# Kernel tuning notes

Hardware: AMD Instinct MI355X
Metric: run time of the kernel (lower is better)

Reference implementation:

```python
import jax, jax.numpy as jnp
import numpy as np

EPS = 1e-5

def conv1x1(x, w, b):
    # x: [B,C,H,W], w: [O,C], b: [O]
    return jnp.einsum('bchw,oc->bohw', x, w) + b[None, :, None, None]

def bn_eval(x, w, b, m, v):
    inv = w / jnp.sqrt(v + EPS)
    return (x - m[None, :, None, None]) * inv[None, :, None, None] + b[None, :, None, None]

def setup_inputs() -> dict:
    key = jax.random.key(0)
    ks = jax.random.split(key, 32)
    B, Fg, Fl, Fi, H, W = 4, 128, 128, 64, 64, 64
    d = {}
    d['g'] = jax.random.normal(ks[0], (B, Fg, H, W), jnp.float32)
    d['x'] = jax.random.normal(ks[1], (B, Fl, H, W), jnp.float32)
    d['wg_w'] = jax.random.normal(ks[2], (Fi, Fg), jnp.float32) * 0.1
    d['wg_b'] = jax.random.normal(ks[3], (Fi,), jnp.float32) * 0.1
    d['bng_w'] = jax.random.uniform(ks[4], (Fi,), jnp.float32)
    d['bng_b'] = jax.random.normal(ks[5], (Fi,), jnp.float32) * 0.1
    d['bng_m'] = jax.random.normal(ks[6], (Fi,), jnp.float32) * 0.1
    d['bng_v'] = jax.random.uniform(ks[7], (Fi,), jnp.float32) + 0.5
    d['wx_w'] = jax.random.normal(ks[8], (Fi, Fl), jnp.float32) * 0.1
    d['wx_b'] = jax.random.normal(ks[9], (Fi,), jnp.float32) * 0.1
    d['bnx_w'] = jax.random.uniform(ks[10], (Fi,), jnp.float32)
    d['bnx_b'] = jax.random.normal(ks[11], (Fi,), jnp.float32) * 0.1
    d['bnx_m'] = jax.random.normal(ks[12], (Fi,), jnp.float32) * 0.1
    d['bnx_v'] = jax.random.uniform(ks[13], (Fi,), jnp.float32) + 0.5
    d['q_w'] = jax.random.normal(ks[14], (Fi // 8, Fi), jnp.float32) * 0.1
    d['q_b'] = jax.random.normal(ks[15], (Fi // 8,), jnp.float32) * 0.1
    d['k_w'] = jax.random.normal(ks[16], (Fi // 8, Fi), jnp.float32) * 0.1
    d['k_b'] = jax.random.normal(ks[17], (Fi // 8,), jnp.float32) * 0.1
    d['v_w'] = jax.random.normal(ks[18], (Fi, Fi), jnp.float32) * 0.1
    d['v_b'] = jax.random.normal(ks[19], (Fi,), jnp.float32) * 0.1
    d['sa_gamma'] = jax.random.normal(ks[20], (1,), jnp.float32)
    d['psi_w'] = jax.random.normal(ks[21], (1, Fi), jnp.float32) * 0.1
    d['psi_b'] = jax.random.normal(ks[22], (1,), jnp.float32) * 0.1
    d['bnp_w'] = jax.random.uniform(ks[23], (1,), jnp.float32)
    d['bnp_b'] = jax.random.normal(ks[24], (1,), jnp.float32) * 0.1
    d['bnp_m'] = jax.random.normal(ks[25], (1,), jnp.float32) * 0.1
    d['bnp_v'] = jax.random.uniform(ks[26], (1,), jnp.float32) + 0.5
    return d

def reference(g, x, wg_w, wg_b, bng_w, bng_b, bng_m, bng_v,
              wx_w, wx_b, bnx_w, bnx_b, bnx_m, bnx_v,
              q_w, q_b, k_w, k_b, v_w, v_b, sa_gamma,
              psi_w, psi_b, bnp_w, bnp_b, bnp_m, bnp_v):
    g1 = bn_eval(conv1x1(g, wg_w, wg_b), bng_w, bng_b, bng_m, bng_v)
    x1 = bn_eval(conv1x1(x, wx_w, wx_b), bnx_w, bnx_b, bnx_m, bnx_v)
    c = jax.nn.relu(g1 + x1)  # [B, Fi, H, W]
    B, C, H, W = c.shape
    N = H * W
    q = conv1x1(c, q_w, q_b).reshape(B, -1, N)  # [B, Fi/8, N]
    k = conv1x1(c, k_w, k_b).reshape(B, -1, N)
    v = conv1x1(c, v_w, v_b).reshape(B, C, N)
    energy = jnp.einsum('bcn,bcm->bnm', q, k)    # [B, N, N]
    attn = jax.nn.softmax(energy, axis=-1)
    sa_out = jnp.einsum('bcm,bnm->bcn', v, attn).reshape(B, C, H, W)
    attended = sa_gamma[0] * sa_out + c
    psi = jax.nn.sigmoid(bn_eval(conv1x1(attended, psi_w, psi_b), bnp_w, bnp_b, bnp_m, bnp_v))
    return x * psi
```

## Files before the change

kernel.cpp:

```cpp
#include <hip/hip_runtime.h>
#include <hip/hip_bf16.h>


typedef short bf16x8 __attribute__((ext_vector_type(8)));
typedef unsigned short u16x8 __attribute__((ext_vector_type(8)));
typedef unsigned short u16x4 __attribute__((ext_vector_type(4)));
typedef float f32x4 __attribute__((ext_vector_type(4)));

__device__ __forceinline__ unsigned short f2b(float f) {
  unsigned u = __builtin_bit_cast(unsigned, f);
  u = (u + 0x7FFFu + ((u >> 16) & 1u)) >> 16;
  return (unsigned short)u;
}
__device__ __forceinline__ unsigned short f2b16(float f) {
  return __builtin_bit_cast(unsigned short, __float2bfloat16(f));
}
__device__ __forceinline__ float b2f(unsigned short u) {
  return __bfloat162float(__builtin_bit_cast(__hip_bfloat16, u));
}

#define EPSV 1e-5f

#define WCAT_OFF   0u
#define WQKV_OFF   32768u
#define BIASC_OFF  44032u
#define BIASQ_OFF  44288u
#define PSIW_OFF   44608u
#define SCAL_OFF   44864u
#define C_OFF      45056u
#define Q_OFF      (C_OFF + 2097152u)
#define K_OFF      (Q_OFF + 262144u)
#define V_OFF      (K_OFF + 262144u)
#define OPART_OFF  (V_OFF + 2097152u)
#define ML_OFF     (OPART_OFF + 16777216u)

__global__ __launch_bounds__(256) void prep_kernel(
    const float* __restrict__ wg_w, const float* __restrict__ wg_b,
    const float* __restrict__ bng_w, const float* __restrict__ bng_b,
    const float* __restrict__ bng_m, const float* __restrict__ bng_v,
    const float* __restrict__ wx_w, const float* __restrict__ wx_b,
    const float* __restrict__ bnx_w, const float* __restrict__ bnx_b,
    const float* __restrict__ bnx_m, const float* __restrict__ bnx_v,
    const float* __restrict__ q_w, const float* __restrict__ q_b,
    const float* __restrict__ k_w, const float* __restrict__ k_b,
    const float* __restrict__ v_w, const float* __restrict__ v_b,
    const float* __restrict__ psi_w, const float* __restrict__ psi_b,
    const float* __restrict__ bnp_w, const float* __restrict__ bnp_b,
    const float* __restrict__ bnp_m, const float* __restrict__ bnp_v,
    const float* __restrict__ sa_gamma,
    unsigned short* __restrict__ Wcat, unsigned short* __restrict__ Wqkv,
    float* __restrict__ bias_c, float* __restrict__ bias_q,
    float* __restrict__ psi_w2, float* __restrict__ scal)
{
  const int t = threadIdx.x;
  const int bid = blockIdx.x;
  if (bid < 16) {
    int o = bid * 4 + (t >> 6);
    int k = (t & 63) * 4;
    float inv;
    const float* src;
    if (k < 128) {
      inv = bng_w[o] * rsqrtf(bng_v[o] + EPSV);
      src = wg_w + o * 128 + k;
    } else {
      inv = bnx_w[o] * rsqrtf(bnx_v[o] + EPSV);
      src = wx_w + o * 128 + (k - 128);
    }
    float4 wv = *(const float4*)src;
    u16x4 pk;
    pk[0] = f2b(wv.x * inv); pk[1] = f2b(wv.y * inv);
    pk[2] = f2b(wv.z * inv); pk[3] = f2b(wv.w * inv);
    *(u16x4*)(Wcat + o * 256 + k) = pk;
    return;
  }
  for (int idx = t; idx < 80 * 64; idx += 256) {
    int r = idx >> 6, k = idx & 63;
    float wv;
    if (r < 8)       wv = q_w[r * 64 + k];
    else if (r < 16) wv = k_w[(r - 8) * 64 + k];
    else             wv = v_w[(r - 16) * 64 + k];
    Wqkv[idx] = f2b(wv);
  }
  if (t < 64) {
    int o = t;
    float invg = bng_w[o] * rsqrtf(bng_v[o] + EPSV);
    float invx = bnx_w[o] * rsqrtf(bnx_v[o] + EPSV);
    bias_c[o] = (wg_b[o] - bng_m[o]) * invg + bng_b[o]
              + (wx_b[o] - bnx_m[o]) * invx + bnx_b[o];
    float invp = bnp_w[0] * rsqrtf(bnp_v[0] + EPSV);
    psi_w2[o] = psi_w[o] * invp;
  }
  if (t < 80)
    bias_q[t] = (t < 8) ? q_b[t] : (t < 16 ? k_b[t - 8] : v_b[t - 16]);
  if (t == 0) {
    float invp = bnp_w[0] * rsqrtf(bnp_v[0] + EPSV);
    scal[0] = sa_gamma[0];
    scal[1] = (psi_b[0] - bnp_m[0]) * invp + bnp_b[0];
  }
}

__global__ __launch_bounds__(256) void conv_qkv_kernel(
    const float* __restrict__ g, const float* __restrict__ x,
    const unsigned short* __restrict__ Wcat, const unsigned short* __restrict__ Wqkv,
    const float* __restrict__ bias_c, const float* __restrict__ bias_q,
    unsigned short* __restrict__ cb, unsigned short* __restrict__ Qb,
    unsigned short* __restrict__ Kb, unsigned short* __restrict__ Vb)
{
  __shared__ __attribute__((aligned(16))) unsigned short xt[16][264];
  __shared__ __attribute__((aligned(16))) unsigned short clds[16][72];
  __shared__ __attribute__((aligned(16))) unsigned short vstage[64][20];

  const int t = threadIdx.x;
  const int bid = blockIdx.x;
  const int b = bid >> 8;
  const int n0 = (bid & 255) << 4;

  {
    const int col4 = t & 3;
    const int rowg = t >> 2;
    float4 v[4];
    #pragma unroll
    for (int rr = 0; rr < 4; ++rr) {
      int row = rowg * 4 + rr;
      const float* src = (row < 128)
          ? (g + ((size_t)(b * 128 + row)) * 4096 + n0 + col4 * 4)
          : (x + ((size_t)(b * 128 + (row - 128))) * 4096 + n0 + col4 * 4);
      v[rr] = *(const float4*)src;
    }
    #pragma unroll
    for (int j = 0; j < 4; ++j) {
      u16x4 pk;
      #pragma unroll
      for (int rr = 0; rr < 4; ++rr)
        pk[rr] = f2b16(((const float*)&v[rr])[j]);
      *(u16x4*)(&xt[col4 * 4 + j][rowg * 4]) = pk;
    }
  }
  __syncthreads();

  const int l = t & 63, w = t >> 6;
  const int l15 = l & 15, lg = l >> 4;
  f32x4 zf = {0.f, 0.f, 0.f, 0.f};

  f32x4 acc = zf;
  const int orow = w * 16 + l15;
  #pragma unroll
  for (int ks = 0; ks < 8; ++ks) {
    bf16x8 af = *(const bf16x8*)(Wcat + orow * 256 + ks * 32 + lg * 8);
    bf16x8 bfv = *(const bf16x8*)(&xt[l15][ks * 32 + lg * 8]);
    acc = __builtin_amdgcn_mfma_f32_16x16x32_bf16(af, bfv, acc, 0, 0, 0);
  }
  #pragma unroll
  for (int r = 0; r < 4; ++r) {
    int o = w * 16 + lg * 4 + r;
    float cv = fmaxf(acc[r] + bias_c[o], 0.f);
    unsigned short cv16 = f2b16(cv);
    cb[((size_t)(b * 64 + o)) * 4096 + n0 + l15] = cv16;
    clds[l15][o] = cv16;
  }
  __syncthreads();

  const int ngl = n0 + l15;
  #pragma unroll
  for (int i = 0; i < 2; ++i) {
    int t5 = w + 4 * i;
    if (t5 >= 5) break;
    f32x4 a2 = zf;
    #pragma unroll
    for (int kk = 0; kk < 2; ++kk) {
      bf16x8 af = *(const bf16x8*)(Wqkv + (t5 * 16 + l15) * 64 + kk * 32 + lg * 8);
      bf16x8 bfv = *(const bf16x8*)(&clds[l15][kk * 32 + lg * 8]);
      a2 = __builtin_amdgcn_mfma_f32_16x16x32_bf16(af, bfv, a2, 0, 0, 0);
    }
    if (t5 == 0) {
      u16x4 pk;
      #pragma unroll
      for (int r = 0; r < 4; ++r)
        pk[r] = f2b16(a2[r] + bias_q[lg * 4 + r]);
      if (lg < 2)
        *(u16x4*)(Qb + (((size_t)b << 12) + ngl) * 8 + lg * 4) = pk;
      else
        *(u16x4*)(Kb + (((size_t)b << 12) + ngl) * 8 + (lg - 2) * 4) = pk;
    } else {
      #pragma unroll
      for (int r = 0; r < 4; ++r) {
        int row = t5 * 16 + lg * 4 + r;
        int vch = row - 16;
        vstage[vch][l15] = f2b16(a2[r] + bias_q[row]);
      }
    }
  }
  __syncthreads();

  {
    int row = t >> 2, seg = t & 3;
    u16x4 pv = *(const u16x4*)(&vstage[row][seg * 4]);
    *(u16x4*)(Vb + ((size_t)(b * 64 + row)) * 4096 + n0 + seg * 4) = pv;
  }
}

__global__ __launch_bounds__(256) void attn_partial_kernel(
    const unsigned short* __restrict__ Qb, const unsigned short* __restrict__ Kb,
    const unsigned short* __restrict__ Vb,
    unsigned short* __restrict__ Opart, float* __restrict__ ml)
{
  __shared__ __attribute__((aligned(16))) unsigned short klds[64][8];
  __shared__ __attribute__((aligned(16))) unsigned short vlds[64][72];
  __shared__ __attribute__((aligned(16))) unsigned short plds[4][16][72];

  const int t = threadIdx.x;
  const int bid = blockIdx.x;
  const int qt = bid & 63;
  const int b = (bid >> 6) & 3;
  const int ci = bid >> 8;
  const int n0 = qt << 6;
  const int l = t & 63, w = t >> 6;
  const int l15 = l & 15, lg = l >> 4;

  bf16x8 qf = {0, 0, 0, 0, 0, 0, 0, 0};
  if (lg == 0)
    qf = *(const bf16x8*)(Qb + (((size_t)b << 12) + n0 + w * 16 + l15) * 8);

  f32x4 zf = {0.f, 0.f, 0.f, 0.f};
  f32x4 O[4];
  O[0] = O[1] = O[2] = O[3] = zf;
  float m_run[4] = {-INFINITY, -INFINITY, -INFINITY, -INFINITY};
  float l_run[4] = {0.f, 0.f, 0.f, 0.f};

  const int m_lo = ci << 9, m_hi = (ci + 1) << 9;
  for (int m0 = m_lo; m0 < m_hi; m0 += 64) {
    if (t < 64)
      *(int4*)(&klds[t][0]) = *(const int4*)(Kb + (((size_t)b << 12) + m0 + t) * 8);
    #pragma unroll
    for (int i = 0; i < 2; ++i) {
      int ci2 = t + 256 * i;
      int row = ci2 >> 3, off = ci2 & 7;
      *(int4*)(&vlds[row][off * 8]) =
          *(const int4*)(Vb + ((size_t)(b * 64 + row)) * 4096 + m0 + off * 8);
    }
    __syncthreads();

    f32x4 e[4];
    #pragma unroll
    for (int mt = 0; mt < 4; ++mt) {
      bf16x8 kf = *(const bf16x8*)(&klds[mt * 16 + l15][0]);
      e[mt] = __builtin_amdgcn_mfma_f32_16x16x32_bf16(qf, kf, zf, 0, 0, 0);
    }

    #pragma unroll
    for (int r = 0; r < 4; ++r) {
      float vm = fmaxf(fmaxf(e[0][r], e[1][r]), fmaxf(e[2][r], e[3][r]));
      vm = fmaxf(vm, __shfl_xor(vm, 1));
      vm = fmaxf(vm, __shfl_xor(vm, 2));
      vm = fmaxf(vm, __shfl_xor(vm, 4));
      vm = fmaxf(vm, __shfl_xor(vm, 8));
      float nm = fmaxf(m_run[r], vm);
      float sc = __expf(m_run[r] - nm);
      float s = 0.f;
      #pragma unroll
      for (int mt = 0; mt < 4; ++mt) {
        float p = __expf(e[mt][r] - nm);
        e[mt][r] = p;
        s += p;
      }
      s += __shfl_xor(s, 1);
      s += __shfl_xor(s, 2);
      s += __shfl_xor(s, 4);
      s += __shfl_xor(s, 8);
      l_run[r] = l_run[r] * sc + s;
      m_run[r] = nm;
      #pragma unroll
      for (int mt = 0; mt < 4; ++mt)
        plds[w][lg * 4 + r][mt * 16 + l15] = f2b16(e[mt][r]);
      #pragma unroll
      for (int ct = 0; ct < 4; ++ct) O[ct][r] *= sc;
    }

    #pragma unroll
    for (int ct = 0; ct < 4; ++ct) {
      #pragma unroll
      for (int kk = 0; kk < 2; ++kk) {
        bf16x8 pa = *(const bf16x8*)(&plds[w][l15][kk * 32 + lg * 8]);
        bf16x8 vb = *(const bf16x8*)(&vlds[ct * 16 + l15][kk * 32 + lg * 8]);
        O[ct] = __builtin_amdgcn_mfma_f32_16x16x32_bf16(pa, vb, O[ct], 0, 0, 0);
      }
    }
    __syncthreads();
  }

  const size_t pb = ((size_t)(ci * 4 + b)) << 12;
  #pragma unroll
  for (int ct = 0; ct < 4; ++ct) {
    int ch = ct * 16 + l15;
    #pragma unroll
    for (int r = 0; r < 4; ++r) {
      int qg = n0 + w * 16 + lg * 4 + r;
      Opart[(pb + qg) * 64 + ch] = f2b16(O[ct][r]);
    }
  }
  if (l15 == 0) {
    #pragma unroll
    for (int r = 0; r < 4; ++r) {
      int qg = n0 + w * 16 + lg * 4 + r;
      float2 mv;
      mv.x = m_run[r]; mv.y = l_run[r];
      *(float2*)(ml + (pb + qg) * 2) = mv;
    }
  }
}

__global__ __launch_bounds__(256) void combine_kernel(
    const unsigned short* __restrict__ Opart, const float* __restrict__ ml,
    const unsigned short* __restrict__ cb, const float* __restrict__ xin,
    const float* __restrict__ psi_w2, const float* __restrict__ scal,
    float* __restrict__ out)
{
  __shared__ __attribute__((aligned(16))) unsigned short c_lds[64][20];
  __shared__ __attribute__((aligned(8))) float2 ml_lds[16][8];
  __shared__ float psi_lds[16];

  const int t = threadIdx.x;
  const int bid = blockIdx.x;
  const int b = bid >> 8;
  const int n0 = (bid & 255) << 4;

  {
    int row = t >> 2, seg = t & 3;
    *(u16x4*)(&c_lds[row][seg * 4]) =
        *(const u16x4*)(cb + ((size_t)(b * 64 + row)) * 4096 + n0 + seg * 4);
  }
  if (t < 128) {
    int q = t >> 3, ci = t & 7;
    ml_lds[q][ci] = *(const float2*)(ml + ((((size_t)(ci * 4 + b)) << 12) + n0 + q) * 2);
  }
  __syncthreads();

  const int q = t >> 4, cg = t & 15;
  const int qg = n0 + q;

  float M = -INFINITY;
  #pragma unroll
  for (int ci = 0; ci < 8; ++ci) M = fmaxf(M, ml_lds[q][ci].x);
  float L = 0.f, wgt[8];
  #pragma unroll
  for (int ci = 0; ci < 8; ++ci) {
    wgt[ci] = __expf(ml_lds[q][ci].x - M);
    L += wgt[ci] * ml_lds[q][ci].y;
  }
  float o4[4] = {0.f, 0.f, 0.f, 0.f};
  #pragma unroll
  for (int ci = 0; ci < 8; ++ci) {
    u16x4 p = *(const u16x4*)(Opart + ((((size_t)(ci * 4 + b)) << 12) + qg) * 64 + cg * 4);
    float wv = wgt[ci];
    #pragma unroll
    for (int k = 0; k < 4; ++k) o4[k] += wv * b2f(p[k]);
  }
  const float invL = 1.f / L;
  const float gamma = scal[0], psi_c = scal[1];
  float ps = 0.f;
  #pragma unroll
  for (int k = 0; k < 4; ++k) {
    int ch = cg * 4 + k;
    ps += psi_w2[ch] * (gamma * (o4[k] * invL) + b2f(c_lds[ch][q]));
  }
  ps += __shfl_xor(ps, 1);
  ps += __shfl_xor(ps, 2);
  ps += __shfl_xor(ps, 4);
  ps += __shfl_xor(ps, 8);
  if (cg == 0)
    psi_lds[q] = 1.f / (1.f + __expf(-(ps + psi_c)));
  __syncthreads();

  #pragma unroll
  for (int i = 0; i < 2; ++i) {
    int idx = t + 256 * i;
    int f = idx >> 2, c4 = idx & 3;
    size_t off = ((size_t)(b * 128 + f)) * 4096 + n0 + c4 * 4;
    float4 xv = *(const float4*)(xin + off);
    float4 ov;
    ov.x = xv.x * psi_lds[c4 * 4 + 0];
    ov.y = xv.y * psi_lds[c4 * 4 + 1];
    ov.z = xv.z * psi_lds[c4 * 4 + 2];
    ov.w = xv.w * psi_lds[c4 * 4 + 3];
    *(float4*)(out + off) = ov;
  }
}

extern "C" void kernel_launch(void* const* d_in, const int* in_sizes, int n_in,
                              void* d_out, int out_size, void* d_ws, size_t ws_size,
                              hipStream_t stream) {
  (void)in_sizes; (void)n_in; (void)out_size; (void)ws_size;
  const float* g     = (const float*)d_in[0];
  const float* x     = (const float*)d_in[1];
  const float* wg_w  = (const float*)d_in[2];
  const float* wg_b  = (const float*)d_in[3];
  const float* bng_w = (const float*)d_in[4];
  const float* bng_b = (const float*)d_in[5];
  const float* bng_m = (const float*)d_in[6];
  const float* bng_v = (const float*)d_in[7];
  const float* wx_w  = (const float*)d_in[8];
  const float* wx_b  = (const float*)d_in[9];
  const float* bnx_w = (const float*)d_in[10];
  const float* bnx_b = (const float*)d_in[11];
  const float* bnx_m = (const float*)d_in[12];
  const float* bnx_v = (const float*)d_in[13];
  const float* q_w   = (const float*)d_in[14];
  const float* q_b   = (const float*)d_in[15];
  const float* k_w   = (const float*)d_in[16];
  const float* k_b   = (const float*)d_in[17];
  const float* v_w   = (const float*)d_in[18];
  const float* v_b   = (const float*)d_in[19];
  const float* sa_g  = (const float*)d_in[20];
  const float* psi_w = (const float*)d_in[21];
  const float* psi_b = (const float*)d_in[22];
  const float* bnp_w = (const float*)d_in[23];
  const float* bnp_b = (const float*)d_in[24];
  const float* bnp_m = (const float*)d_in[25];
  const float* bnp_v = (const float*)d_in[26];
  float* out = (float*)d_out;

  char* ws = (char*)d_ws;
  unsigned short* Wcat = (unsigned short*)(ws + WCAT_OFF);
  unsigned short* Wqkv = (unsigned short*)(ws + WQKV_OFF);
  float* bias_c = (float*)(ws + BIASC_OFF);
  float* bias_q = (float*)(ws + BIASQ_OFF);
  float* psiw2  = (float*)(ws + PSIW_OFF);
  float* scal   = (float*)(ws + SCAL_OFF);
  unsigned short* cb = (unsigned short*)(ws + C_OFF);
  unsigned short* Qb = (unsigned short*)(ws + Q_OFF);
  unsigned short* Kb = (unsigned short*)(ws + K_OFF);
  unsigned short* Vb = (unsigned short*)(ws + V_OFF);
  unsigned short* Opart = (unsigned short*)(ws + OPART_OFF);
  float* mlb   = (float*)(ws + ML_OFF);

  hipLaunchKernelGGL(prep_kernel, dim3(17), dim3(256), 0, stream,
                     wg_w, wg_b, bng_w, bng_b, bng_m, bng_v,
                     wx_w, wx_b, bnx_w, bnx_b, bnx_m, bnx_v,
                     q_w, q_b, k_w, k_b, v_w, v_b,
                     psi_w, psi_b, bnp_w, bnp_b, bnp_m, bnp_v, sa_g,
                     Wcat, Wqkv, bias_c, bias_q, psiw2, scal);

  hipLaunchKernelGGL(conv_qkv_kernel, dim3(1024), dim3(256), 0, stream,
                     g, x, Wcat, Wqkv, bias_c, bias_q, cb, Qb, Kb, Vb);

  hipLaunchKernelGGL(attn_partial_kernel, dim3(2048), dim3(256), 0, stream,
                     Qb, Kb, Vb, Opart, mlb);

  hipLaunchKernelGGL(combine_kernel, dim3(1024), dim3(256), 0, stream,
                     Opart, mlb, cb, x, psiw2, scal, out);
}
```

Measured before the change: 185.6 us.

## Fold weight prep into conv kernel, use exp2 softmax with lazy rescaling

Removes the separate prep kernel, so each conv block loads the fp32 weights, applies the BN scale and converts to bf16 in registers, and computes the folded biases inline. Q is pre-scaled by log2(e) so the softmax and the combine step can use the hardware exp2 instruction. The online softmax now skips the running-max update and the O rescale unless some row's new max exceeds the old one by more than 8. The cost is redundant weight conversion in every one of the 1024 conv blocks, plus a small numeric risk from the deferred max.

New measurement: 193.5 us. 4.3% more time.

```diff
diff --git a/kernel.cpp b/kernel.cpp
--- a/kernel.cpp
+++ b/kernel.cpp
@@ -7,11 +7,6 @@
 typedef unsigned short u16x4 __attribute__((ext_vector_type(4)));
 typedef float f32x4 __attribute__((ext_vector_type(4)));
 
-__device__ __forceinline__ unsigned short f2b(float f) {
-  unsigned u = __builtin_bit_cast(unsigned, f);
-  u = (u + 0x7FFFu + ((u >> 16) & 1u)) >> 16;
-  return (unsigned short)u;
-}
 __device__ __forceinline__ unsigned short f2b16(float f) {
   return __builtin_bit_cast(unsigned short, __float2bfloat16(f));
 }
@@ -20,21 +15,17 @@
 }
 
 #define EPSV 1e-5f
-
-#define WCAT_OFF   0u
-#define WQKV_OFF   32768u
-#define BIASC_OFF  44032u
-#define BIASQ_OFF  44288u
-#define PSIW_OFF   44608u
-#define SCAL_OFF   44864u
-#define C_OFF      45056u
+#define LOG2E 1.44269504088896340736f
+
+#define C_OFF      0u
 #define Q_OFF      (C_OFF + 2097152u)
 #define K_OFF      (Q_OFF + 262144u)
 #define V_OFF      (K_OFF + 262144u)
 #define OPART_OFF  (V_OFF + 2097152u)
 #define ML_OFF     (OPART_OFF + 16777216u)
 
-__global__ __launch_bounds__(256) void prep_kernel(
+__global__ __launch_bounds__(256) void conv_fused_kernel(
+    const float* __restrict__ g, const float* __restrict__ x,
     const float* __restrict__ wg_w, const float* __restrict__ wg_b,
     const float* __restrict__ bng_w, const float* __restrict__ bng_b,
     const float* __restrict__ bng_m, const float* __restrict__ bng_v,
@@ -44,65 +35,6 @@
     const float* __restrict__ q_w, const float* __restrict__ q_b,
     const float* __restrict__ k_w, const float* __restrict__ k_b,
     const float* __restrict__ v_w, const float* __restrict__ v_b,
-    const float* __restrict__ psi_w, const float* __restrict__ psi_b,
-    const float* __restrict__ bnp_w, const float* __restrict__ bnp_b,
-    const float* __restrict__ bnp_m, const float* __restrict__ bnp_v,
-    const float* __restrict__ sa_gamma,
-    unsigned short* __restrict__ Wcat, unsigned short* __restrict__ Wqkv,
-    float* __restrict__ bias_c, float* __restrict__ bias_q,
-    float* __restrict__ psi_w2, float* __restrict__ scal)
-{
-  const int t = threadIdx.x;
-  const int bid = blockIdx.x;
-  if (bid < 16) {
-    int o = bid * 4 + (t >> 6);
-    int k = (t & 63) * 4;
-    float inv;
-    const float* src;
-    if (k < 128) {
-      inv = bng_w[o] * rsqrtf(bng_v[o] + EPSV);
-      src = wg_w + o * 128 + k;
-    } else {
-      inv = bnx_w[o] * rsqrtf(bnx_v[o] + EPSV);
-      src = wx_w + o * 128 + (k - 128);
-    }
-    float4 wv = *(const float4*)src;
-    u16x4 pk;
-    pk[0] = f2b(wv.x * inv); pk[1] = f2b(wv.y * inv);
-    pk[2] = f2b(wv.z * inv); pk[3] = f2b(wv.w * inv);
-    *(u16x4*)(Wcat + o * 256 + k) = pk;
-    return;
-  }
-  for (int idx = t; idx < 80 * 64; idx += 256) {
-    int r = idx >> 6, k = idx & 63;
-    float wv;
-    if (r < 8)       wv = q_w[r * 64 + k];
-    else if (r < 16) wv = k_w[(r - 8) * 64 + k];
-    else             wv = v_w[(r - 16) * 64 + k];
-    Wqkv[idx] = f2b(wv);
-  }
-  if (t < 64) {
-    int o = t;
-    float invg = bng_w[o] * rsqrtf(bng_v[o] + EPSV);
-    float invx = bnx_w[o] * rsqrtf(bnx_v[o] + EPSV);
-    bias_c[o] = (wg_b[o] - bng_m[o]) * invg + bng_b[o]
-              + (wx_b[o] - bnx_m[o]) * invx + bnx_b[o];
-    float invp = bnp_w[0] * rsqrtf(bnp_v[0] + EPSV);
-    psi_w2[o] = psi_w[o] * invp;
-  }
-  if (t < 80)
-    bias_q[t] = (t < 8) ? q_b[t] : (t < 16 ? k_b[t - 8] : v_b[t - 16]);
-  if (t == 0) {
-    float invp = bnp_w[0] * rsqrtf(bnp_v[0] + EPSV);
-    scal[0] = sa_gamma[0];
-    scal[1] = (psi_b[0] - bnp_m[0]) * invp + bnp_b[0];
-  }
-}
-
-__global__ __launch_bounds__(256) void conv_qkv_kernel(
-    const float* __restrict__ g, const float* __restrict__ x,
-    const unsigned short* __restrict__ Wcat, const unsigned short* __restrict__ Wqkv,
-    const float* __restrict__ bias_c, const float* __restrict__ bias_q,
     unsigned short* __restrict__ cb, unsigned short* __restrict__ Qb,
     unsigned short* __restrict__ Kb, unsigned short* __restrict__ Vb)
 {
@@ -136,24 +68,47 @@
       *(u16x4*)(&xt[col4 * 4 + j][rowg * 4]) = pk;
     }
   }
-  __syncthreads();
 
   const int l = t & 63, w = t >> 6;
   const int l15 = l & 15, lg = l >> 4;
   f32x4 zf = {0.f, 0.f, 0.f, 0.f};
 
+  const int orow = w * 16 + l15;
+  const float invg = bng_w[orow] * rsqrtf(bng_v[orow] + EPSV);
+  const float invx = bnx_w[orow] * rsqrtf(bnx_v[orow] + EPSV);
+  bf16x8 afrag[8];
+  #pragma unroll
+  for (int ks = 0; ks < 8; ++ks) {
+    int k = ks * 32 + lg * 8;
+    const float* wp;
+    float sc;
+    if (k < 128) { wp = wg_w + orow * 128 + k;         sc = invg; }
+    else         { wp = wx_w + orow * 128 + (k - 128); sc = invx; }
+    float4 w0 = *(const float4*)wp;
+    float4 w1 = *(const float4*)(wp + 4);
+    u16x8 pk;
+    pk[0] = f2b16(w0.x * sc); pk[1] = f2b16(w0.y * sc);
+    pk[2] = f2b16(w0.z * sc); pk[3] = f2b16(w0.w * sc);
+    pk[4] = f2b16(w1.x * sc); pk[5] = f2b16(w1.y * sc);
+    pk[6] = f2b16(w1.z * sc); pk[7] = f2b16(w1.w * sc);
+    afrag[ks] = __builtin_bit_cast(bf16x8, pk);
+  }
+  __syncthreads();
+
   f32x4 acc = zf;
-  const int orow = w * 16 + l15;
   #pragma unroll
   for (int ks = 0; ks < 8; ++ks) {
-    bf16x8 af = *(const bf16x8*)(Wcat + orow * 256 + ks * 32 + lg * 8);
     bf16x8 bfv = *(const bf16x8*)(&xt[l15][ks * 32 + lg * 8]);
-    acc = __builtin_amdgcn_mfma_f32_16x16x32_bf16(af, bfv, acc, 0, 0, 0);
+    acc = __builtin_amdgcn_mfma_f32_16x16x32_bf16(afrag[ks], bfv, acc, 0, 0, 0);
   }
   #pragma unroll
   for (int r = 0; r < 4; ++r) {
     int o = w * 16 + lg * 4 + r;
-    float cv = fmaxf(acc[r] + bias_c[o], 0.f);
+    float ig = bng_w[o] * rsqrtf(bng_v[o] + EPSV);
+    float ix = bnx_w[o] * rsqrtf(bnx_v[o] + EPSV);
+    float bc = (wg_b[o] - bng_m[o]) * ig + bng_b[o]
+             + (wx_b[o] - bnx_m[o]) * ix + bnx_b[o];
+    float cv = fmaxf(acc[r] + bc, 0.f);
     unsigned short cv16 = f2b16(cv);
     cb[((size_t)(b * 64 + o)) * 4096 + n0 + l15] = cv16;
     clds[l15][o] = cv16;
@@ -165,18 +120,35 @@
   for (int i = 0; i < 2; ++i) {
     int t5 = w + 4 * i;
     if (t5 >= 5) break;
+    int wrow = t5 * 16 + l15;
     f32x4 a2 = zf;
     #pragma unroll
     for (int kk = 0; kk < 2; ++kk) {
-      bf16x8 af = *(const bf16x8*)(Wqkv + (t5 * 16 + l15) * 64 + kk * 32 + lg * 8);
-      bf16x8 bfv = *(const bf16x8*)(&clds[l15][kk * 32 + lg * 8]);
-      a2 = __builtin_amdgcn_mfma_f32_16x16x32_bf16(af, bfv, a2, 0, 0, 0);
+      int k = kk * 32 + lg * 8;
+      const float* wp = (wrow < 8)  ? (q_w + wrow * 64 + k)
+                      : (wrow < 16) ? (k_w + (wrow - 8) * 64 + k)
+                                    : (v_w + (wrow - 16) * 64 + k);
+      float4 w0 = *(const float4*)wp;
+      float4 w1 = *(const float4*)(wp + 4);
+      u16x8 pk;
+      pk[0] = f2b16(w0.x); pk[1] = f2b16(w0.y);
+      pk[2] = f2b16(w0.z); pk[3] = f2b16(w0.w);
+      pk[4] = f2b16(w1.x); pk[5] = f2b16(w1.y);
+      pk[6] = f2b16(w1.z); pk[7] = f2b16(w1.w);
+      bf16x8 bfv = *(const bf16x8*)(&clds[l15][k]);
+      a2 = __builtin_amdgcn_mfma_f32_16x16x32_bf16(
+          __builtin_bit_cast(bf16x8, pk), bfv, a2, 0, 0, 0);
     }
     if (t5 == 0) {
       u16x4 pk;
       #pragma unroll
-      for (int r = 0; r < 4; ++r)
-        pk[r] = f2b16(a2[r] + bias_q[lg * 4 + r]);
+      for (int r = 0; r < 4; ++r) {
+        int row = lg * 4 + r;
+        float val;
+        if (row < 8) val = (a2[r] + q_b[row]) * LOG2E;
+        else         val = a2[r] + k_b[row - 8];
+        pk[r] = f2b16(val);
+      }
       if (lg < 2)
         *(u16x4*)(Qb + (((size_t)b << 12) + ngl) * 8 + lg * 4) = pk;
       else
@@ -184,9 +156,8 @@
     } else {
       #pragma unroll
       for (int r = 0; r < 4; ++r) {
-        int row = t5 * 16 + lg * 4 + r;
-        int vch = row - 16;
-        vstage[vch][l15] = f2b16(a2[r] + bias_q[row]);
+        int vch = (t5 - 1) * 16 + lg * 4 + r;
+        vstage[vch][l15] = f2b16(a2[r] + v_b[vch]);
       }
     }
   }
@@ -254,12 +225,12 @@
       vm = fmaxf(vm, __shfl_xor(vm, 2));
       vm = fmaxf(vm, __shfl_xor(vm, 4));
       vm = fmaxf(vm, __shfl_xor(vm, 8));
-      float nm = fmaxf(m_run[r], vm);
-      float sc = __expf(m_run[r] - nm);
+      bool nosk = !__all(vm <= m_run[r] + 8.f);
+      float nm = nosk ? fmaxf(m_run[r], vm) : m_run[r];
       float s = 0.f;
       #pragma unroll
       for (int mt = 0; mt < 4; ++mt) {
-        float p = __expf(e[mt][r] - nm);
+        float p = __builtin_amdgcn_exp2f(e[mt][r] - nm);
         e[mt][r] = p;
         s += p;
       }
@@ -267,13 +238,18 @@
       s += __shfl_xor(s, 2);
       s += __shfl_xor(s, 4);
       s += __shfl_xor(s, 8);
-      l_run[r] = l_run[r] * sc + s;
-      m_run[r] = nm;
+      if (nosk) {
+        float sc = __builtin_amdgcn_exp2f(m_run[r] - nm);
+        l_run[r] = l_run[r] * sc + s;
+        m_run[r] = nm;
+        #pragma unroll
+        for (int ct = 0; ct < 4; ++ct) O[ct][r] *= sc;
+      } else {
+        l_run[r] += s;
+      }
       #pragma unroll
       for (int mt = 0; mt < 4; ++mt)
         plds[w][lg * 4 + r][mt * 16 + l15] = f2b16(e[mt][r]);
-      #pragma unroll
-      for (int ct = 0; ct < 4; ++ct) O[ct][r] *= sc;
     }
 
     #pragma unroll
@@ -312,7 +288,10 @@
 __global__ __launch_bounds__(256) void combine_kernel(
     const unsigned short* __restrict__ Opart, const float* __restrict__ ml,
     const unsigned short* __restrict__ cb, const float* __restrict__ xin,
-    const float* __restrict__ psi_w2, const float* __restrict__ scal,
+    const float* __restrict__ psi_w, const float* __restrict__ psi_b,
+    const float* __restrict__ bnp_w, const float* __restrict__ bnp_b,
+    const float* __restrict__ bnp_m, const float* __restrict__ bnp_v,
+    const float* __restrict__ sa_gamma,
     float* __restrict__ out)
 {
   __shared__ __attribute__((aligned(16))) unsigned short c_lds[64][20];
@@ -335,6 +314,10 @@
   }
   __syncthreads();
 
+  const float invp = bnp_w[0] * rsqrtf(bnp_v[0] + EPSV);
+  const float psi_c = (psi_b[0] - bnp_m[0]) * invp + bnp_b[0];
+  const float gamma = sa_gamma[0];
+
   const int q = t >> 4, cg = t & 15;
   const int qg = n0 + q;
 
@@ -344,7 +327,7 @@
   float L = 0.f, wgt[8];
   #pragma unroll
   for (int ci = 0; ci < 8; ++ci) {
-    wgt[ci] = __expf(ml_lds[q][ci].x - M);
+    wgt[ci] = __builtin_amdgcn_exp2f(ml_lds[q][ci].x - M);
     L += wgt[ci] * ml_lds[q][ci].y;
   }
   float o4[4] = {0.f, 0.f, 0.f, 0.f};
@@ -356,12 +339,11 @@
     for (int k = 0; k < 4; ++k) o4[k] += wv * b2f(p[k]);
   }
   const float invL = 1.f / L;
-  const float gamma = scal[0], psi_c = scal[1];
   float ps = 0.f;
   #pragma unroll
   for (int k = 0; k < 4; ++k) {
     int ch = cg * 4 + k;
-    ps += psi_w2[ch] * (gamma * (o4[k] * invL) + b2f(c_lds[ch][q]));
+    ps += (psi_w[ch] * invp) * (gamma * (o4[k] * invL) + b2f(c_lds[ch][q]));
   }
   ps += __shfl_xor(ps, 1);
   ps += __shfl_xor(ps, 2);
@@ -420,32 +402,24 @@
   float* out = (float*)d_out;
 
   char* ws = (char*)d_ws;
-  unsigned short* Wcat = (unsigned short*)(ws + WCAT_OFF);
-  unsigned short* Wqkv = (unsigned short*)(ws + WQKV_OFF);
-  float* bias_c = (float*)(ws + BIASC_OFF);
-  float* bias_q = (float*)(ws + BIASQ_OFF);
-  float* psiw2  = (float*)(ws + PSIW_OFF);
-  float* scal   = (float*)(ws + SCAL_OFF);
   unsigned short* cb = (unsigned short*)(ws + C_OFF);
   unsigned short* Qb = (unsigned short*)(ws + Q_OFF);
   unsigned short* Kb = (unsigned short*)(ws + K_OFF);
   unsigned short* Vb = (unsigned short*)(ws + V_OFF);
   unsigned short* Opart = (unsigned short*)(ws + OPART_OFF);
-  float* mlb   = (float*)(ws + ML_OFF);
-
-  hipLaunchKernelGGL(prep_kernel, dim3(17), dim3(256), 0, stream,
-                     wg_w, wg_b, bng_w, bng_b, bng_m, bng_v,
+  float* mlb = (float*)(ws + ML_OFF);
+
+  hipLaunchKernelGGL(conv_fused_kernel, dim3(1024), dim3(256), 0, stream,
+                     g, x, wg_w, wg_b, bng_w, bng_b, bng_m, bng_v,
                      wx_w, wx_b, bnx_w, bnx_b, bnx_m, bnx_v,
                      q_w, q_b, k_w, k_b, v_w, v_b,
-                     psi_w, psi_b, bnp_w, bnp_b, bnp_m, bnp_v, sa_g,
-                     Wcat, Wqkv, bias_c, bias_q, psiw2, scal);
-
-  hipLaunchKernelGGL(conv_qkv_kernel, dim3(1024), dim3(256), 0, stream,
-                     g, x, Wcat, Wqkv, bias_c, bias_q, cb, Qb, Kb, Vb);
+                     cb, Qb, Kb, Vb);
 
   hipLaunchKernelGGL(attn_partial_kernel, dim3(2048), dim3(256), 0, stream,
                      Qb, Kb, Vb, Opart, mlb);
 
   hipLaunchKernelGGL(combine_kernel, dim3(1024), dim3(256), 0, stream,
-                     Opart, mlb, cb, x, psiw2, scal, out);
-}
+                     Opart, mlb, cb, x,
+                     psi_w, psi_b, bnp_w, bnp_b, bnp_m, bnp_v, sa_g,
+                     out);
+}
```
